# Kernel tuning notes

Hardware: AMD Instinct MI355X
Metric: run time of the kernel (lower is better)

Reference implementation:

```python
import jax, jax.numpy as jnp
import numpy as np

HIDDEN = 768
NUM_HEADS = 12
HEAD_SIZE = HIDDEN // NUM_HEADS
LN_EPS = 1e-5


def setup_inputs() -> dict:
    key = jax.random.key(0)
    ks = jax.random.split(key, 10)
    B, S, H = 2, 4096, HIDDEN
    std = 1.0 / np.sqrt(H)
    inp = {
        "hidden_states": jax.random.normal(ks[0], (B, S, H), dtype=jnp.float32),
        "attention_mask": jnp.ones((B, S), dtype=jnp.float32),
        "Wq": jax.random.normal(ks[1], (H, H), dtype=jnp.float32) * std,
        "bq": jnp.zeros((H,), dtype=jnp.float32),
        "Wk": jax.random.normal(ks[2], (H, H), dtype=jnp.float32) * std,
        "bk": jnp.zeros((H,), dtype=jnp.float32),
        "Wv": jax.random.normal(ks[3], (H, H), dtype=jnp.float32) * std,
        "bv": jnp.zeros((H,), dtype=jnp.float32),
        "Wo": jax.random.normal(ks[4], (H, H), dtype=jnp.float32) * std,
        "bo": jnp.zeros((H,), dtype=jnp.float32),
        "ln_gamma": jnp.ones((H,), dtype=jnp.float32),
        "ln_beta": jnp.zeros((H,), dtype=jnp.float32),
    }
    return inp


def _split_heads(x):
    # [B, S, H] -> [B, nH, S, hd]
    B, S, _ = x.shape
    return x.reshape(B, S, NUM_HEADS, HEAD_SIZE).transpose(0, 2, 1, 3)


def reference(hidden_states, attention_mask, Wq, bq, Wk, bk, Wv, bv, Wo, bo, ln_gamma, ln_beta):
    # QKV projections (torch Linear: x @ W.T + b; here W is stored as [in, out])
    q = _split_heads(hidden_states @ Wq + bq)
    k = _split_heads(hidden_states @ Wk + bk)
    v = _split_heads(hidden_states @ Wv + bv)

    scores = jnp.einsum("bhqd,bhkd->bhqk", q, k) / jnp.sqrt(jnp.float32(HEAD_SIZE))
    # additive mask: (1 - mask) * -10000, broadcast over heads and query positions
    scores = scores + (1.0 - attention_mask)[:, None, None, :] * -10000.0
    probs = jax.nn.softmax(scores, axis=-1)  # dropout_prob = 0 -> identity

    ctx = jnp.einsum("bhqk,bhkd->bhqd", probs, v)
    B, _, S, _ = ctx.shape
    ctx = ctx.transpose(0, 2, 1, 3).reshape(B, S, HIDDEN)

    out = ctx @ Wo + bo
    resid = out + hidden_states
    mu = jnp.mean(resid, axis=-1, keepdims=True)
    var = jnp.var(resid, axis=-1, keepdims=True)
    return (resid - mu) * jax.lax.rsqrt(var + LN_EPS) * ln_gamma + ln_beta
```

## Files before the change

kernel.cpp:

```cpp
#include <hip/hip_runtime.h>
#include <hip/hip_bf16.h>

#define HID 768
#define NHEADS 12
#define HDIM 64
#define SEQ 4096
#define BB 2
#define MTOT (BB * SEQ)

typedef __attribute__((ext_vector_type(8))) short bf16x8;
typedef __attribute__((ext_vector_type(16))) float f32x16;

#define LOG2E 1.4426950408889634f

__device__ inline unsigned pack2bf(float a, float b) {
    __hip_bfloat162 h = __float22bfloat162_rn(float2{a, b});
    return *(unsigned*)&h;
}

__global__ __launch_bounds__(256) void cast_x_kernel(
    const float* __restrict__ X, __hip_bfloat16* __restrict__ Xb)
{
    const size_t i = ((size_t)blockIdx.x * 256 + threadIdx.x) * 8;
    const float4 x0 = *(const float4*)(X + i);
    const float4 x1 = *(const float4*)(X + i + 4);
    unsigned u[4];
    u[0] = pack2bf(x0.x, x0.y);
    u[1] = pack2bf(x0.z, x0.w);
    u[2] = pack2bf(x1.x, x1.y);
    u[3] = pack2bf(x1.z, x1.w);
    *(uint4*)(Xb + i) = *(uint4*)u;
}

__global__ __launch_bounds__(256) void pack_w_kernel(
    const float* __restrict__ Wq, const float* __restrict__ Wk,
    const float* __restrict__ Wv, const float* __restrict__ Wo,
    __hip_bfloat16* __restrict__ Wt)
{
    const int z = blockIdx.z;
    const float* __restrict__ W = (z == 0) ? Wq : (z == 1) ? Wk : (z == 2) ? Wv : Wo;
    const int in0  = blockIdx.x * 64;
    const int out0 = blockIdx.y * 64;
    const int t = threadIdx.x;

    __shared__ float T[64][65];
#pragma unroll
    for (int i = 0; i < 4; ++i) {
        const int idx = t + 256 * i;
        const int row = idx >> 4;
        const int c4  = (idx & 15) << 2;
        const float4 v = *(const float4*)(W + (size_t)(in0 + row) * HID + out0 + c4);
        T[row][c4 + 0] = v.x; T[row][c4 + 1] = v.y;
        T[row][c4 + 2] = v.z; T[row][c4 + 3] = v.w;
    }
    __syncthreads();

    const int o  = t >> 2;
    const int cb = (t & 3) << 4;
    __hip_bfloat16 tmp[16];
#pragma unroll
    for (int k = 0; k < 16; ++k)
        tmp[k] = __float2bfloat16(T[cb + k][o]);
    __hip_bfloat16* __restrict__ dst =
        Wt + (size_t)(z * HID + out0 + o) * HID + in0 + cb;
    *(uint4*)(dst)     = *(uint4*)(&tmp[0]);
    *(uint4*)(dst + 8) = *(uint4*)(&tmp[8]);
}

#define GSTAGE(ASB, BSB, BUF, APTR, BPTR, K0) do {                                 \
    _Pragma("unroll")                                                              \
    for (int j_ = 0; j_ < 4; ++j_) {                                               \
        const __hip_bfloat16* ga_ = (APTR) + (size_t)(r0 + 32 * j_) * HID + (K0) + csw; \
        const __hip_bfloat16* gb_ = (BPTR) + (size_t)(r0 + 32 * j_) * HID + (K0) + csw; \
        __builtin_amdgcn_global_load_lds(                                          \
            (const __attribute__((address_space(1))) unsigned*)ga_,                \
            (__attribute__((address_space(3))) unsigned*)(&ASB[BUF][0][0] + (256 * j_ + 64 * w) * 8), 16, 0, 0); \
        __builtin_amdgcn_global_load_lds(                                          \
            (const __attribute__((address_space(1))) unsigned*)gb_,                \
            (__attribute__((address_space(3))) unsigned*)(&BSB[BUF][0][0] + (256 * j_ + 64 * w) * 8), 16, 0, 0); \
    }                                                                              \
} while (0)

#define GTILE(ASB, BSB, BUF) do {                                                  \
    _Pragma("unroll")                                                              \
    for (int kh = 0; kh < 4; ++kh) {                                               \
        const int sc = ((2 * kh + g) ^ (col & 7)) << 3;                            \
        const bf16x8 a0 = *(const bf16x8*)&ASB[BUF][64 * wm + col][sc];            \
        const bf16x8 a1 = *(const bf16x8*)&ASB[BUF][64 * wm + 32 + col][sc];       \
        const bf16x8 b0 = *(const bf16x8*)&BSB[BUF][64 * wn + col][sc];            \
        const bf16x8 b1 = *(const bf16x8*)&BSB[BUF][64 * wn + 32 + col][sc];       \
        acc[0][0] = __builtin_amdgcn_mfma_f32_32x32x16_bf16(a0, b0, acc[0][0], 0, 0, 0); \
        acc[0][1] = __builtin_amdgcn_mfma_f32_32x32x16_bf16(a0, b1, acc[0][1], 0, 0, 0); \
        acc[1][0] = __builtin_amdgcn_mfma_f32_32x32x16_bf16(a1, b0, acc[1][0], 0, 0, 0); \
        acc[1][1] = __builtin_amdgcn_mfma_f32_32x32x16_bf16(a1, b1, acc[1][1], 0, 0, 0); \
    }                                                                              \
} while (0)

__global__ __launch_bounds__(256) void qkv_mfma_kernel(
    const __hip_bfloat16* __restrict__ Xb, const __hip_bfloat16* __restrict__ Wt,
    const float* __restrict__ bq, const float* __restrict__ bk,
    const float* __restrict__ bv,
    __hip_bfloat16* __restrict__ Qo, __hip_bfloat16* __restrict__ Ko,
    __hip_bfloat16* __restrict__ Vo)
{
    const int nblk = blockIdx.x;
    const int z  = nblk / 6;
    const int f0 = (nblk % 6) * 128;
    const int n0 = nblk * 128;
    const int m0 = blockIdx.y * 128;

    const float* __restrict__ bias = (z == 0) ? bq : (z == 1) ? bk : bv;

    const int t    = threadIdx.x;
    const int w    = t >> 6;
    const int lane = t & 63;
    const int col  = lane & 31;
    const int g    = lane >> 5;
    const int wm   = w & 1;
    const int wn   = w >> 1;

    __shared__ __hip_bfloat16 smem[4 * 128 * 64];
    __hip_bfloat16 (*Asb)[128][64] = (__hip_bfloat16(*)[128][64])smem;
    __hip_bfloat16 (*Bsb)[128][64] = (__hip_bfloat16(*)[128][64])(smem + 2 * 128 * 64);

    const int r0  = t >> 3;
    const int csw = (((t & 7) ^ (r0 & 7)) << 3);

    const __hip_bfloat16* __restrict__ Am = Xb + (size_t)m0 * HID;
    const __hip_bfloat16* __restrict__ Bn = Wt + (size_t)n0 * HID;

    f32x16 acc[2][2];
#pragma unroll
    for (int mt = 0; mt < 2; ++mt)
#pragma unroll
        for (int nt = 0; nt < 2; ++nt)
#pragma unroll
            for (int r = 0; r < 16; ++r) acc[mt][nt][r] = 0.f;

    GSTAGE(Asb, Bsb, 0, Am, Bn, 0);
    __syncthreads();
    for (int k0 = 0; k0 < HID; k0 += 128) {
        GSTAGE(Asb, Bsb, 1, Am, Bn, k0 + 64);
        GTILE(Asb, Bsb, 0);
        __syncthreads();
        if (k0 + 128 < HID) GSTAGE(Asb, Bsb, 0, Am, Bn, k0 + 128);
        GTILE(Asb, Bsb, 1);
        __syncthreads();
    }

    if (z < 2) {
        __hip_bfloat16* __restrict__ Out = (z == 0) ? Qo : Ko;
        const int h = (f0 >> 6) + wn;
#pragma unroll
        for (int mt = 0; mt < 2; ++mt)
#pragma unroll
            for (int nt = 0; nt < 2; ++nt) {
                const int d = 32 * nt + col;
                const float bsv = bias[f0 + 64 * wn + d];
#pragma unroll
                for (int r = 0; r < 16; ++r) {
                    const int m = m0 + 64 * wm + 32 * mt + (r & 3) + 8 * (r >> 2) + 4 * g;
                    const int b = m >> 12;
                    const int s = m & (SEQ - 1);
                    Out[(((size_t)(b * NHEADS + h)) * SEQ + s) * HDIM + d] =
                        __float2bfloat16(acc[mt][nt][r] + bsv);
                }
            }
    } else {
        __syncthreads();
        __hip_bfloat16 (*Ts)[136] = (__hip_bfloat16(*)[136])smem;
#pragma unroll
        for (int mt = 0; mt < 2; ++mt)
#pragma unroll
            for (int nt = 0; nt < 2; ++nt) {
                const int nloc = 64 * wn + 32 * nt + col;
                const float bsv = bias[f0 + nloc];
#pragma unroll
                for (int rg = 0; rg < 4; ++rg) {
                    const int mbase = 64 * wm + 32 * mt + 8 * rg + 4 * g;
                    unsigned pu[2];
                    pu[0] = pack2bf(acc[mt][nt][4 * rg + 0] + bsv,
                                    acc[mt][nt][4 * rg + 1] + bsv);
                    pu[1] = pack2bf(acc[mt][nt][4 * rg + 2] + bsv,
                                    acc[mt][nt][4 * rg + 3] + bsv);
                    *(uint2*)&Ts[nloc][mbase] = *(uint2*)pu;
                }
            }
        __syncthreads();
        const int nloc = t >> 1;
        const int half = t & 1;
        const int hh = (f0 >> 6) + (nloc >> 6);
        const int d  = nloc & 63;
        const int bb = m0 >> 12;
        const int s0 = m0 & (SEQ - 1);
        __hip_bfloat16* __restrict__ dst =
            Vo + (((size_t)(bb * NHEADS + hh)) * HDIM + d) * SEQ + s0 + 64 * half;
        const __hip_bfloat16* srcp = &Ts[nloc][64 * half];
#pragma unroll
        for (int j = 0; j < 8; ++j)
            *(uint4*)(dst + 8 * j) = *(const uint4*)(srcp + 8 * j);
    }
}

typedef __attribute__((ext_vector_type(2))) unsigned uswap2;

__global__ __launch_bounds__(256, 2) void attn_kernel(
    const __hip_bfloat16* __restrict__ Qb, const __hip_bfloat16* __restrict__ Kb,
    const __hip_bfloat16* __restrict__ Vt, const float* __restrict__ mask,
    __hip_bfloat16* __restrict__ Op, float* __restrict__ lp)
{
    const int bh = blockIdx.y;
    const int b  = bh / NHEADS;
    const int h  = bh - b * NHEADS;
    const int kspan = SEQ / gridDim.z;
    const int kbeg  = blockIdx.z * kspan;

    const int t    = threadIdx.x;
    const int w    = t >> 6;
    const int lane = t & 63;
    const int col  = lane & 31;
    const int g    = lane >> 5;
    const int qw   = blockIdx.x * 256 + 64 * w;

    __shared__ __hip_bfloat16 Ksb[2][64][64];
    __shared__ __hip_bfloat16 Vsb[2][64][64];
    __shared__ float madd[2048];

    const __hip_bfloat16* __restrict__ Qh = Qb + (size_t)bh * SEQ * HDIM;
    const __hip_bfloat16* __restrict__ Kh = Kb + (size_t)bh * SEQ * HDIM;
    const __hip_bfloat16* __restrict__ Vh = Vt + (size_t)bh * HDIM * SEQ;

    for (int j = t; j < kspan; j += 256)
        madd[j] = (1.0f - mask[b * SEQ + kbeg + j]) * (-10000.0f * LOG2E);

    const int r0  = t >> 3;
    const int csw = (((t & 7) ^ (r0 & 7)) << 3);

#define STAGE(BUF, KT) do {                                                        \
    const __hip_bfloat16* gk0_ = Kh + (size_t)((KT) + r0) * HDIM + csw;            \
    const __hip_bfloat16* gk1_ = Kh + (size_t)((KT) + r0 + 32) * HDIM + csw;       \
    const __hip_bfloat16* gv0_ = Vh + (size_t)r0 * SEQ + (KT) + csw;               \
    const __hip_bfloat16* gv1_ = Vh + (size_t)(r0 + 32) * SEQ + (KT) + csw;        \
    __hip_bfloat16* lk_ = &Ksb[BUF][0][0] + w * 512;                               \
    __hip_bfloat16* lv_ = &Vsb[BUF][0][0] + w * 512;                               \
    __builtin_amdgcn_global_load_lds(                                              \
        (const __attribute__((address_space(1))) unsigned*)gk0_,                   \
        (__attribute__((address_space(3))) unsigned*)lk_, 16, 0, 0);               \
    __builtin_amdgcn_global_load_lds(                                              \
        (const __attribute__((address_space(1))) unsigned*)gk1_,                   \
        (__attribute__((address_space(3))) unsigned*)(lk_ + 2048), 16, 0, 0);      \
    __builtin_amdgcn_global_load_lds(                                              \
        (const __attribute__((address_space(1))) unsigned*)gv0_,                   \
        (__attribute__((address_space(3))) unsigned*)lv_, 16, 0, 0);               \
    __builtin_amdgcn_global_load_lds(                                              \
        (const __attribute__((address_space(1))) unsigned*)gv1_,                   \
        (__attribute__((address_space(3))) unsigned*)(lv_ + 2048), 16, 0, 0);      \
} while (0)

    bf16x8 bq[2][4];
#pragma unroll
    for (int mt = 0; mt < 2; ++mt)
#pragma unroll
        for (int kh = 0; kh < 4; ++kh)
            bq[mt][kh] = *(const bf16x8*)(Qh + (size_t)(qw + 32 * mt + col) * HDIM
                                          + 16 * kh + 8 * g);

    f32x16 O[2][2];
    float lac[2] = {0.f, 0.f};
#pragma unroll
    for (int mt = 0; mt < 2; ++mt)
#pragma unroll
        for (int dt = 0; dt < 2; ++dt)
#pragma unroll
            for (int r = 0; r < 16; ++r) O[mt][dt][r] = 0.f;

    const float kscale = 0.125f * LOG2E;

#define ATTN_TILE(BUF, KT0) do {                                                   \
    f32x16 St[2][2];                                                               \
    _Pragma("unroll")                                                              \
    for (int mt = 0; mt < 2; ++mt)                                                 \
        _Pragma("unroll")                                                          \
        for (int nt = 0; nt < 2; ++nt)                                             \
            _Pragma("unroll")                                                      \
            for (int r = 0; r < 16; ++r) St[mt][nt][r] = 0.f;                      \
    _Pragma("unroll")                                                              \
    for (int kh = 0; kh < 4; ++kh) {                                               \
        const int sc = ((2 * kh + g) ^ (col & 7)) << 3;                            \
        const bf16x8 ak0 = *(const bf16x8*)&Ksb[BUF][col][sc];                     \
        const bf16x8 ak1 = *(const bf16x8*)&Ksb[BUF][32 + col][sc];                \
        St[0][0] = __builtin_amdgcn_mfma_f32_32x32x16_bf16(ak0, bq[0][kh], St[0][0], 0, 0, 0); \
        St[1][0] = __builtin_amdgcn_mfma_f32_32x32x16_bf16(ak0, bq[1][kh], St[1][0], 0, 0, 0); \
        St[0][1] = __builtin_amdgcn_mfma_f32_32x32x16_bf16(ak1, bq[0][kh], St[0][1], 0, 0, 0); \
        St[1][1] = __builtin_amdgcn_mfma_f32_32x32x16_bf16(ak1, bq[1][kh], St[1][1], 0, 0, 0); \
    }                                                                              \
    _Pragma("unroll")                                                              \
    for (int mt = 0; mt < 2; ++mt) {                                               \
        unsigned g4x[2][4], g4y[2][4];                                             \
        _Pragma("unroll")                                                          \
        for (int nt = 0; nt < 2; ++nt) {                                           \
            _Pragma("unroll")                                                      \
            for (int b4 = 0; b4 < 4; ++b4) {                                       \
                const float4 mm = *(const float4*)&madd[(KT0) + 32 * nt + 8 * b4 + 4 * g]; \
                const float p0 = __builtin_amdgcn_exp2f(fmaf(St[mt][nt][4 * b4 + 0], kscale, mm.x)); \
                const float p1 = __builtin_amdgcn_exp2f(fmaf(St[mt][nt][4 * b4 + 1], kscale, mm.y)); \
                const float p2 = __builtin_amdgcn_exp2f(fmaf(St[mt][nt][4 * b4 + 2], kscale, mm.z)); \
                const float p3 = __builtin_amdgcn_exp2f(fmaf(St[mt][nt][4 * b4 + 3], kscale, mm.w)); \
                lac[mt] += (p0 + p1) + (p2 + p3);                                  \
                g4x[nt][b4] = pack2bf(p0, p1);                                     \
                g4y[nt][b4] = pack2bf(p2, p3);                                     \
            }                                                                      \
        }                                                                          \
        _Pragma("unroll")                                                          \
        for (int kh = 0; kh < 4; ++kh) {                                           \
            const int nt  = kh >> 1;                                               \
            const int khl = kh & 1;                                                \
            union { unsigned u[4]; bf16x8 v; } au;                                 \
            ATTN_PTRANS(au, g4x[nt][2 * khl], g4x[nt][2 * khl + 1],                \
                            g4y[nt][2 * khl], g4y[nt][2 * khl + 1]);               \
            const int sc = ((2 * kh + g) ^ (col & 7)) << 3;                        \
            const bf16x8 bv0 = *(const bf16x8*)&Vsb[BUF][col][sc];                 \
            const bf16x8 bv1 = *(const bf16x8*)&Vsb[BUF][32 + col][sc];            \
            O[mt][0] = __builtin_amdgcn_mfma_f32_32x32x16_bf16(au.v, bv0, O[mt][0], 0, 0, 0); \
            O[mt][1] = __builtin_amdgcn_mfma_f32_32x32x16_bf16(au.v, bv1, O[mt][1], 0, 0, 0); \
        }                                                                          \
    }                                                                              \
} while (0)

#if __has_builtin(__builtin_amdgcn_permlane32_swap)
#define ATTN_PTRANS(au, lox, hix, loy, hiy) do {                                   \
    uswap2 sx_ = __builtin_amdgcn_permlane32_swap((lox), (hix), false, false);     \
    uswap2 sy_ = __builtin_amdgcn_permlane32_swap((loy), (hiy), false, false);     \
    au.u[0] = sx_[0]; au.u[1] = sy_[0]; au.u[2] = sx_[1]; au.u[3] = sy_[1];        \
} while (0)
#else
#define ATTN_PTRANS(au, lox, hix, loy, hiy) do {                                   \
    const unsigned sxv_ = g ? (lox) : (hix);                                       \
    const unsigned syv_ = g ? (loy) : (hiy);                                       \
    const unsigned rx_ = (unsigned)__shfl_xor((int)sxv_, 32, 64);                  \
    const unsigned ry_ = (unsigned)__shfl_xor((int)syv_, 32, 64);                  \
    if (g) { au.u[0] = rx_;   au.u[1] = ry_;   au.u[2] = (hix); au.u[3] = (hiy); } \
    else   { au.u[0] = (lox); au.u[1] = (loy); au.u[2] = rx_;   au.u[3] = ry_;  }  \
} while (0)
#endif

    STAGE(0, kbeg);
    __syncthreads();

    for (int kt0 = 0; kt0 < kspan; kt0 += 128) {
        STAGE(1, kbeg + kt0 + 64);
        ATTN_TILE(0, kt0);
        __syncthreads();
        if (kt0 + 128 < kspan) STAGE(0, kbeg + kt0 + 128);
        ATTN_TILE(1, kt0 + 64);
        __syncthreads();
    }
#undef STAGE
#undef ATTN_TILE
#undef ATTN_PTRANS

    const size_t opbase = (size_t)blockIdx.z * ((size_t)MTOT * HID);
#pragma unroll
    for (int mt = 0; mt < 2; ++mt) {
        const float l = lac[mt] + __shfl_xor(lac[mt], 32, 64);
        if (g == 0)
            lp[((size_t)blockIdx.z * (BB * NHEADS) + bh) * SEQ + qw + 32 * mt + col] = l;
#pragma unroll
        for (int dt = 0; dt < 2; ++dt)
#pragma unroll
            for (int r = 0; r < 16; ++r) {
                const int q = qw + 32 * mt + (r & 3) + 8 * (r >> 2) + 4 * g;
                const int d = 32 * dt + col;
                Op[opbase + ((size_t)b * SEQ + q) * HID + h * HDIM + d] =
                    __float2bfloat16(O[mt][dt][r]);
            }
    }
}

__global__ __launch_bounds__(256) void combine_kernel(
    const __hip_bfloat16* __restrict__ Op, const float* __restrict__ lp,
    __hip_bfloat16* __restrict__ Ctx, int KS)
{
    const size_t i = ((size_t)blockIdx.x * 256 + threadIdx.x) * 8;
    const int n   = (int)(i % HID);
    const int row = (int)(i / HID);
    const int h = n >> 6;
    const int b = row >> 12;
    const int q = row & (SEQ - 1);
    const int bh = b * NHEADS + h;

    float denom = 0.f;
    float o[8] = {};
    for (int kz = 0; kz < KS; ++kz) {
        denom += lp[((size_t)kz * (BB * NHEADS) + bh) * SEQ + q];
        uint4 u = *(const uint4*)(Op + (size_t)kz * ((size_t)MTOT * HID) + i);
        const __hip_bfloat16* e = (const __hip_bfloat16*)&u;
#pragma unroll
        for (int j = 0; j < 8; ++j) o[j] += __bfloat162float(e[j]);
    }
    const float inv = 1.0f / denom;
    unsigned u[4];
#pragma unroll
    for (int j = 0; j < 4; ++j)
        u[j] = pack2bf(o[2 * j] * inv, o[2 * j + 1] * inv);
    *(uint4*)(Ctx + i) = *(uint4*)u;
}

__global__ __launch_bounds__(256) void out_mfma_kernel(
    const __hip_bfloat16* __restrict__ Cb, const __hip_bfloat16* __restrict__ Wto,
    const float* __restrict__ bo, const float* __restrict__ X,
    float* __restrict__ Resid)
{
    const int n0 = blockIdx.x * 128;
    const int m0 = blockIdx.y * 128;

    const int t    = threadIdx.x;
    const int w    = t >> 6;
    const int lane = t & 63;
    const int col  = lane & 31;
    const int g    = lane >> 5;
    const int wm   = w & 1;
    const int wn   = w >> 1;

    __shared__ __hip_bfloat16 smem[4 * 128 * 64];
    __hip_bfloat16 (*Asb)[128][64] = (__hip_bfloat16(*)[128][64])smem;
    __hip_bfloat16 (*Bsb)[128][64] = (__hip_bfloat16(*)[128][64])(smem + 2 * 128 * 64);

    const int r0  = t >> 3;
    const int csw = (((t & 7) ^ (r0 & 7)) << 3);

    const __hip_bfloat16* __restrict__ Am = Cb  + (size_t)m0 * HID;
    const __hip_bfloat16* __restrict__ Bn = Wto + (size_t)n0 * HID;

    f32x16 acc[2][2];
#pragma unroll
    for (int mt = 0; mt < 2; ++mt)
#pragma unroll
        for (int nt = 0; nt < 2; ++nt)
#pragma unroll
            for (int r = 0; r < 16; ++r) acc[mt][nt][r] = 0.f;

    GSTAGE(Asb, Bsb, 0, Am, Bn, 0);
    __syncthreads();
    for (int k0 = 0; k0 < HID; k0 += 128) {
        GSTAGE(Asb, Bsb, 1, Am, Bn, k0 + 64);
        GTILE(Asb, Bsb, 0);
        __syncthreads();
        if (k0 + 128 < HID) GSTAGE(Asb, Bsb, 0, Am, Bn, k0 + 128);
        GTILE(Asb, Bsb, 1);
        __syncthreads();
    }

#pragma unroll
    for (int mt = 0; mt < 2; ++mt)
#pragma unroll
        for (int nt = 0; nt < 2; ++nt) {
            const int n = n0 + 64 * wn + 32 * nt + col;
            const float bsv = bo[n];
#pragma unroll
            for (int r = 0; r < 16; ++r) {
                const int m = m0 + 64 * wm + 32 * mt + (r & 3) + 8 * (r >> 2) + 4 * g;
                Resid[(size_t)m * HID + n] = acc[mt][nt][r] + bsv + X[(size_t)m * HID + n];
            }
        }
}

__global__ __launch_bounds__(256) void ln_kernel(
    const float* __restrict__ Rin, const float* __restrict__ gamma,
    const float* __restrict__ beta, float* __restrict__ Out)
{
    const int row = blockIdx.x;
    const int t   = threadIdx.x;
    const float* __restrict__ x = Rin + (size_t)row * HID;

    const float v0 = x[t];
    const float v1 = x[t + 256];
    const float v2 = x[t + 512];
    float s  = v0 + v1 + v2;
    float s2 = v0 * v0 + v1 * v1 + v2 * v2;
#pragma unroll
    for (int off = 32; off; off >>= 1) {
        s  += __shfl_xor(s,  off, 64);
        s2 += __shfl_xor(s2, off, 64);
    }
    __shared__ float rs[4], rs2[4];
    const int w = t >> 6, lane = t & 63;
    if (lane == 0) { rs[w] = s; rs2[w] = s2; }
    __syncthreads();
    const float tot  = rs[0] + rs[1] + rs[2] + rs[3];
    const float tot2 = rs2[0] + rs2[1] + rs2[2] + rs2[3];
    const float mu   = tot * (1.0f / HID);
    const float var  = tot2 * (1.0f / HID) - mu * mu;
    const float rsig = rsqrtf(var + 1e-5f);

    float* __restrict__ y = Out + (size_t)row * HID;
    y[t]       = (v0 - mu) * rsig * gamma[t]       + beta[t];
    y[t + 256] = (v1 - mu) * rsig * gamma[t + 256] + beta[t + 256];
    y[t + 512] = (v2 - mu) * rsig * gamma[t + 512] + beta[t + 512];
}

extern "C" void kernel_launch(void* const* d_in, const int* in_sizes, int n_in,
                              void* d_out, int out_size, void* d_ws, size_t ws_size,
                              hipStream_t stream)
{
    const float* X     = (const float*)d_in[0];
    const float* mask  = (const float*)d_in[1];
    const float* Wq    = (const float*)d_in[2];
    const float* bq    = (const float*)d_in[3];
    const float* Wk    = (const float*)d_in[4];
    const float* bk    = (const float*)d_in[5];
    const float* Wv    = (const float*)d_in[6];
    const float* bv    = (const float*)d_in[7];
    const float* Wo    = (const float*)d_in[8];
    const float* bo    = (const float*)d_in[9];
    const float* gamma = (const float*)d_in[10];
    const float* beta  = (const float*)d_in[11];
    float* out = (float*)d_out;

    const size_t N = (size_t)MTOT * HID;
    const size_t WTE = (size_t)4 * HID * HID;

    char* p = (char*)d_ws;
    __hip_bfloat16* Xb  = (__hip_bfloat16*)p;  p += 2 * N;
    __hip_bfloat16* Wt  = (__hip_bfloat16*)p;  p += 2 * WTE;
    __hip_bfloat16* Qw  = (__hip_bfloat16*)p;  p += 2 * N;
    __hip_bfloat16* Kw  = (__hip_bfloat16*)p;  p += 2 * N;
    __hip_bfloat16* Vtw = (__hip_bfloat16*)p;  p += 2 * N;
    char* opb = p;
    const size_t fixed = (size_t)(opb - (char*)d_ws);

    const size_t lpsz4 = 4 * (size_t)(BB * NHEADS) * SEQ * sizeof(float);
    const int KS = (ws_size >= fixed + 4 * 2 * N + lpsz4) ? 4 : 2;

    __hip_bfloat16* Op  = (__hip_bfloat16*)opb;
    float* lpt = (float*)(opb + (size_t)KS * 2 * N);
    __hip_bfloat16* Ctxb = Xb;
    float* Rd = (float*)Kw;

    cast_x_kernel<<<(int)(N / 2048), 256, 0, stream>>>(X, Xb);
    pack_w_kernel<<<dim3(12, 12, 4), 256, 0, stream>>>(Wq, Wk, Wv, Wo, Wt);
    qkv_mfma_kernel<<<dim3(18, MTOT / 128), 256, 0, stream>>>(
        Xb, Wt, bq, bk, bv, Qw, Kw, Vtw);
    attn_kernel<<<dim3(SEQ / 256, BB * NHEADS, KS), 256, 0, stream>>>(
        Qw, Kw, Vtw, mask, Op, lpt);
    combine_kernel<<<(int)(N / 2048), 256, 0, stream>>>(Op, lpt, Ctxb, KS);
    out_mfma_kernel<<<dim3(6, MTOT / 128), 256, 0, stream>>>(
        Ctxb, Wt + (size_t)2304 * HID, bo, X, Rd);
    ln_kernel<<<MTOT, 256, 0, stream>>>(Rd, gamma, beta, out);
}
```

Baseline: 328.1 us.

## Halve attention query tile per wave to 32 rows, doubling grid size

Each wave in the attention kernel now handles 32 query rows instead of 64, so a block covers 128 queries and the grid doubles along the query axis. This cuts accumulator and score registers roughly in half, and launch bounds now request 3 blocks per CU to raise occupancy. In exchange, every K/V tile staged into LDS is reused by half as many queries, which doubles global K/V traffic and staging work per unit of compute.

New measurement: 332.5 us. About the same (+1.3%).

```diff
diff --git a/kernel.cpp b/kernel.cpp
--- a/kernel.cpp
+++ b/kernel.cpp
@@ -204,7 +204,7 @@
 
 typedef __attribute__((ext_vector_type(2))) unsigned uswap2;
 
-__global__ __launch_bounds__(256, 2) void attn_kernel(
+__global__ __launch_bounds__(256, 3) void attn_kernel(
     const __hip_bfloat16* __restrict__ Qb, const __hip_bfloat16* __restrict__ Kb,
     const __hip_bfloat16* __restrict__ Vt, const float* __restrict__ mask,
     __hip_bfloat16* __restrict__ Op, float* __restrict__ lp)
@@ -220,7 +220,7 @@
     const int lane = t & 63;
     const int col  = lane & 31;
     const int g    = lane >> 5;
-    const int qw   = blockIdx.x * 256 + 64 * w;
+    const int qw   = blockIdx.x * 128 + 32 * w;
 
     __shared__ __hip_bfloat16 Ksb[2][64][64];
     __shared__ __hip_bfloat16 Vsb[2][64][64];
@@ -257,73 +257,61 @@
         (__attribute__((address_space(3))) unsigned*)(lv_ + 2048), 16, 0, 0);      \
 } while (0)
 
-    bf16x8 bq[2][4];
-#pragma unroll
-    for (int mt = 0; mt < 2; ++mt)
-#pragma unroll
-        for (int kh = 0; kh < 4; ++kh)
-            bq[mt][kh] = *(const bf16x8*)(Qh + (size_t)(qw + 32 * mt + col) * HDIM
-                                          + 16 * kh + 8 * g);
-
-    f32x16 O[2][2];
-    float lac[2] = {0.f, 0.f};
-#pragma unroll
-    for (int mt = 0; mt < 2; ++mt)
-#pragma unroll
-        for (int dt = 0; dt < 2; ++dt)
-#pragma unroll
-            for (int r = 0; r < 16; ++r) O[mt][dt][r] = 0.f;
+    bf16x8 bq[4];
+#pragma unroll
+    for (int kh = 0; kh < 4; ++kh)
+        bq[kh] = *(const bf16x8*)(Qh + (size_t)(qw + col) * HDIM + 16 * kh + 8 * g);
+
+    f32x16 O[2];
+    float lac = 0.f;
+#pragma unroll
+    for (int dt = 0; dt < 2; ++dt)
+#pragma unroll
+        for (int r = 0; r < 16; ++r) O[dt][r] = 0.f;
 
     const float kscale = 0.125f * LOG2E;
 
 #define ATTN_TILE(BUF, KT0) do {                                                   \
-    f32x16 St[2][2];                                                               \
+    f32x16 St[2];                                                                  \
     _Pragma("unroll")                                                              \
-    for (int mt = 0; mt < 2; ++mt)                                                 \
+    for (int nt = 0; nt < 2; ++nt)                                                 \
         _Pragma("unroll")                                                          \
-        for (int nt = 0; nt < 2; ++nt)                                             \
-            _Pragma("unroll")                                                      \
-            for (int r = 0; r < 16; ++r) St[mt][nt][r] = 0.f;                      \
+        for (int r = 0; r < 16; ++r) St[nt][r] = 0.f;                              \
     _Pragma("unroll")                                                              \
     for (int kh = 0; kh < 4; ++kh) {                                               \
         const int sc = ((2 * kh + g) ^ (col & 7)) << 3;                            \
         const bf16x8 ak0 = *(const bf16x8*)&Ksb[BUF][col][sc];                     \
         const bf16x8 ak1 = *(const bf16x8*)&Ksb[BUF][32 + col][sc];                \
-        St[0][0] = __builtin_amdgcn_mfma_f32_32x32x16_bf16(ak0, bq[0][kh], St[0][0], 0, 0, 0); \
-        St[1][0] = __builtin_amdgcn_mfma_f32_32x32x16_bf16(ak0, bq[1][kh], St[1][0], 0, 0, 0); \
-        St[0][1] = __builtin_amdgcn_mfma_f32_32x32x16_bf16(ak1, bq[0][kh], St[0][1], 0, 0, 0); \
-        St[1][1] = __builtin_amdgcn_mfma_f32_32x32x16_bf16(ak1, bq[1][kh], St[1][1], 0, 0, 0); \
+        St[0] = __builtin_amdgcn_mfma_f32_32x32x16_bf16(ak0, bq[kh], St[0], 0, 0, 0); \
+        St[1] = __builtin_amdgcn_mfma_f32_32x32x16_bf16(ak1, bq[kh], St[1], 0, 0, 0); \
+    }                                                                              \
+    unsigned g4x[2][4], g4y[2][4];                                                 \
+    _Pragma("unroll")                                                              \
+    for (int nt = 0; nt < 2; ++nt) {                                               \
+        _Pragma("unroll")                                                          \
+        for (int b4 = 0; b4 < 4; ++b4) {                                           \
+            const float4 mm = *(const float4*)&madd[(KT0) + 32 * nt + 8 * b4 + 4 * g]; \
+            const float p0 = __builtin_amdgcn_exp2f(fmaf(St[nt][4 * b4 + 0], kscale, mm.x)); \
+            const float p1 = __builtin_amdgcn_exp2f(fmaf(St[nt][4 * b4 + 1], kscale, mm.y)); \
+            const float p2 = __builtin_amdgcn_exp2f(fmaf(St[nt][4 * b4 + 2], kscale, mm.z)); \
+            const float p3 = __builtin_amdgcn_exp2f(fmaf(St[nt][4 * b4 + 3], kscale, mm.w)); \
+            lac += (p0 + p1) + (p2 + p3);                                          \
+            g4x[nt][b4] = pack2bf(p0, p1);                                         \
+            g4y[nt][b4] = pack2bf(p2, p3);                                         \
+        }                                                                          \
     }                                                                              \
     _Pragma("unroll")                                                              \
-    for (int mt = 0; mt < 2; ++mt) {                                               \
-        unsigned g4x[2][4], g4y[2][4];                                             \
-        _Pragma("unroll")                                                          \
-        for (int nt = 0; nt < 2; ++nt) {                                           \
-            _Pragma("unroll")                                                      \
-            for (int b4 = 0; b4 < 4; ++b4) {                                       \
-                const float4 mm = *(const float4*)&madd[(KT0) + 32 * nt + 8 * b4 + 4 * g]; \
-                const float p0 = __builtin_amdgcn_exp2f(fmaf(St[mt][nt][4 * b4 + 0], kscale, mm.x)); \
-                const float p1 = __builtin_amdgcn_exp2f(fmaf(St[mt][nt][4 * b4 + 1], kscale, mm.y)); \
-                const float p2 = __builtin_amdgcn_exp2f(fmaf(St[mt][nt][4 * b4 + 2], kscale, mm.z)); \
-                const float p3 = __builtin_amdgcn_exp2f(fmaf(St[mt][nt][4 * b4 + 3], kscale, mm.w)); \
-                lac[mt] += (p0 + p1) + (p2 + p3);                                  \
-                g4x[nt][b4] = pack2bf(p0, p1);                                     \
-                g4y[nt][b4] = pack2bf(p2, p3);                                     \
-            }                                                                      \
-        }                                                                          \
-        _Pragma("unroll")                                                          \
-        for (int kh = 0; kh < 4; ++kh) {                                           \
-            const int nt  = kh >> 1;                                               \
-            const int khl = kh & 1;                                                \
-            union { unsigned u[4]; bf16x8 v; } au;                                 \
-            ATTN_PTRANS(au, g4x[nt][2 * khl], g4x[nt][2 * khl + 1],                \
-                            g4y[nt][2 * khl], g4y[nt][2 * khl + 1]);               \
-            const int sc = ((2 * kh + g) ^ (col & 7)) << 3;                        \
-            const bf16x8 bv0 = *(const bf16x8*)&Vsb[BUF][col][sc];                 \
-            const bf16x8 bv1 = *(const bf16x8*)&Vsb[BUF][32 + col][sc];            \
-            O[mt][0] = __builtin_amdgcn_mfma_f32_32x32x16_bf16(au.v, bv0, O[mt][0], 0, 0, 0); \
-            O[mt][1] = __builtin_amdgcn_mfma_f32_32x32x16_bf16(au.v, bv1, O[mt][1], 0, 0, 0); \
-        }                                                                          \
+    for (int kh = 0; kh < 4; ++kh) {                                               \
+        const int nt  = kh >> 1;                                                   \
+        const int khl = kh & 1;                                                    \
+        union { unsigned u[4]; bf16x8 v; } au;                                     \
+        ATTN_PTRANS(au, g4x[nt][2 * khl], g4x[nt][2 * khl + 1],                    \
+                        g4y[nt][2 * khl], g4y[nt][2 * khl + 1]);                   \
+        const int sc = ((2 * kh + g) ^ (col & 7)) << 3;                            \
+        const bf16x8 bv0 = *(const bf16x8*)&Vsb[BUF][col][sc];                     \
+        const bf16x8 bv1 = *(const bf16x8*)&Vsb[BUF][32 + col][sc];                \
+        O[0] = __builtin_amdgcn_mfma_f32_32x32x16_bf16(au.v, bv0, O[0], 0, 0, 0);  \
+        O[1] = __builtin_amdgcn_mfma_f32_32x32x16_bf16(au.v, bv1, O[1], 0, 0, 0);  \
     }                                                                              \
 } while (0)
 
@@ -360,19 +348,18 @@
 #undef ATTN_PTRANS
 
     const size_t opbase = (size_t)blockIdx.z * ((size_t)MTOT * HID);
-#pragma unroll
-    for (int mt = 0; mt < 2; ++mt) {
-        const float l = lac[mt] + __shfl_xor(lac[mt], 32, 64);
+    {
+        const float l = lac + __shfl_xor(lac, 32, 64);
         if (g == 0)
-            lp[((size_t)blockIdx.z * (BB * NHEADS) + bh) * SEQ + qw + 32 * mt + col] = l;
+            lp[((size_t)blockIdx.z * (BB * NHEADS) + bh) * SEQ + qw + col] = l;
 #pragma unroll
         for (int dt = 0; dt < 2; ++dt)
 #pragma unroll
             for (int r = 0; r < 16; ++r) {
-                const int q = qw + 32 * mt + (r & 3) + 8 * (r >> 2) + 4 * g;
+                const int q = qw + (r & 3) + 8 * (r >> 2) + 4 * g;
                 const int d = 32 * dt + col;
                 Op[opbase + ((size_t)b * SEQ + q) * HID + h * HDIM + d] =
-                    __float2bfloat16(O[mt][dt][r]);
+                    __float2bfloat16(O[dt][r]);
             }
     }
 }
@@ -541,7 +528,7 @@
     pack_w_kernel<<<dim3(12, 12, 4), 256, 0, stream>>>(Wq, Wk, Wv, Wo, Wt);
     qkv_mfma_kernel<<<dim3(18, MTOT / 128), 256, 0, stream>>>(
         Xb, Wt, bq, bk, bv, Qw, Kw, Vtw);
-    attn_kernel<<<dim3(SEQ / 256, BB * NHEADS, KS), 256, 0, stream>>>(
+    attn_kernel<<<dim3(SEQ / 128, BB * NHEADS, KS), 256, 0, stream>>>(
         Qw, Kw, Vtw, mask, Op, lpt);
     combine_kernel<<<(int)(N / 2048), 256, 0, stream>>>(Op, lpt, Ctxb, KS);
     out_mfma_kernel<<<dim3(6, MTOT / 128), 256, 0, stream>>>(
```
